# Kernel tuning notes

Hardware: AMD Instinct MI355X
Metric: run time of the kernel (lower is better)

The kernel has to match this reference:

```python
import jax, jax.numpy as jnp
import numpy as np

B, N, E, H, BS = 8, 8192, 256, 2, 8
D = E // H  # head_dim = 128


def setup_inputs() -> dict:
    key = jax.random.key(0)
    ks = jax.random.split(key, 8)
    s = 0.02
    return {
        "x": jax.random.normal(ks[0], (B, N, E), jnp.float32),
        "Wq": jax.random.normal(ks[1], (E, E), jnp.float32) * s,
        "bq": jnp.zeros((E,), jnp.float32),
        "Wk": jax.random.normal(ks[2], (E, E), jnp.float32) * s,
        "bk": jnp.zeros((E,), jnp.float32),
        "Wv": jax.random.normal(ks[3], (E, E), jnp.float32) * s,
        "bv": jnp.zeros((E,), jnp.float32),
        "P": jax.random.normal(ks[4], (D, D), jnp.float32) / jnp.sqrt(jnp.float32(D)),
    }


def reference(x, Wq, bq, Wk, bk, Wv, bv, P):
    Bx, Nx, Ex = x.shape
    nb = Nx // BS  # number of diagonal blocks
    # Linear projections (torch nn.Linear: y = x @ W^T + b), split heads
    q = (x @ Wq.T + bq).reshape(Bx, Nx, H, D)
    k = (x @ Wk.T + bk).reshape(Bx, Nx, H, D)
    v = (x @ Wv.T + bv).reshape(Bx, Nx, H, D)
    # Shared feature projection on q and k
    q = jnp.einsum('bnhe,ei->bnhi', q, P)
    k = jnp.einsum('bnhe,ei->bnhi', k, P)
    # Block-diagonal attention: off-block scores are -inf in the original,
    # so softmax over the full row == softmax within each block.
    qb = q.reshape(Bx, nb, BS, H, D)
    kb = k.reshape(Bx, nb, BS, H, D)
    vb = v.reshape(Bx, nb, BS, H, D)
    scores = jnp.einsum('bgnhd,bgmhd->bgnhm', qb, kb) / jnp.sqrt(jnp.asarray(D, x.dtype))
    attn = jax.nn.softmax(scores, axis=-1)  # [B, nb, BS, H, BS]
    out = jnp.einsum('bgnhm,bgmhd->bgnhd', attn, vb)
    return out.reshape(Bx, Nx, Ex)
```

## Files before the change

kernel.cpp:

```cpp
#include <hip/hip_runtime.h>


typedef __attribute__((ext_vector_type(8))) short bf16x8;
typedef __attribute__((ext_vector_type(4))) float f32x4;

__device__ __forceinline__ short f2bf(float f) {
  unsigned int u = __builtin_bit_cast(unsigned int, f);
  u = (u + 0x7FFFu + ((u >> 16) & 1u)) >> 16;
  return (short)u;
}
__device__ __forceinline__ float bf2f(short s) {
  unsigned int u = ((unsigned int)(unsigned short)s) << 16;
  return __builtin_bit_cast(float, u);
}
__device__ __forceinline__ int swz(int r) { return ((r ^ (r >> 3)) & 7) << 4; }

__global__ void prep_weights(const float* __restrict__ Wq, const float* __restrict__ bq,
                             const float* __restrict__ Wk, const float* __restrict__ bk,
                             const float* __restrict__ Wv, const float* __restrict__ bv,
                             const float* __restrict__ P,
                             short* __restrict__ WT, float* __restrict__ beff) {
  const int c = blockIdx.x;
  const int e = threadIdx.x;
  float acc = 0.f, bacc = 0.f;
  if (c < 512) {
    const float* W  = (c < 256) ? Wq : Wk;
    const float* bb = (c < 256) ? bq : bk;
    const int cc = c & 255;
    const int h = cc >> 7, i = cc & 127;
    for (int d = 0; d < 128; ++d) {
      const float p = P[d * 128 + i];
      acc += W[(h * 128 + d) * 256 + e] * p;
      if (e == 0) bacc += bb[h * 128 + d] * p;
    }
  } else {
    const int cc = c - 512;
    acc = Wv[cc * 256 + e];
    bacc = bv[cc];
  }
  WT[c * 256 + e] = f2bf(acc);
  if (e == 0) beff[c] = bacc;
}

__global__ __launch_bounds__(512, 4)
void fused_qkv_attn(const float* __restrict__ x, const short* __restrict__ WT,
                    const float* __restrict__ beff, float* __restrict__ out) {
  __shared__ __align__(16) char lds[65536];
  char* const xa = lds;
  char* const qk = lds + 16384;

  const int tid = threadIdx.x;
  const long tok0 = (long)blockIdx.x * 32;

  {
    const int r  = tid >> 4;
    const int kc = (tid & 15) * 16;
    const float4* xp = (const float4*)(x + (tok0 + r) * 256 + kc);
    float4 f0 = xp[0], f1 = xp[1], f2 = xp[2], f3 = xp[3];
    bf16x8 v0, v1;
    v0[0]=f2bf(f0.x); v0[1]=f2bf(f0.y); v0[2]=f2bf(f0.z); v0[3]=f2bf(f0.w);
    v0[4]=f2bf(f1.x); v0[5]=f2bf(f1.y); v0[6]=f2bf(f1.z); v0[7]=f2bf(f1.w);
    v1[0]=f2bf(f2.x); v1[1]=f2bf(f2.y); v1[2]=f2bf(f2.z); v1[3]=f2bf(f2.w);
    v1[4]=f2bf(f3.x); v1[5]=f2bf(f3.y); v1[6]=f2bf(f3.z); v1[7]=f2bf(f3.w);
    *(bf16x8*)(xa + r * 512 + ((kc * 2)       ^ swz(r))) = v0;
    *(bf16x8*)(xa + r * 512 + ((kc * 2 + 16)  ^ swz(r))) = v1;
  }
  __syncthreads();

  const int w = tid >> 6, l = tid & 63;
  const int lrow = l & 15, lk = l >> 4;
  const int nb = w * 96;

  f32x4 acc[2][6];
#pragma unroll
  for (int nf = 0; nf < 6; ++nf) {
    const float bv_ = beff[nb + nf * 16 + lrow];
    acc[0][nf] = (f32x4){bv_, bv_, bv_, bv_};
    acc[1][nf] = acc[0][nf];
  }
#pragma unroll
  for (int ks = 0; ks < 8; ++ks) {
    const int kb = ks * 32;
    bf16x8 a0 = *(const bf16x8*)(xa + lrow        * 512 + ((kb * 2 + lk * 16) ^ swz(lrow)));
    bf16x8 a1 = *(const bf16x8*)(xa + (16 + lrow) * 512 + ((kb * 2 + lk * 16) ^ swz(16 + lrow)));
#pragma unroll
    for (int nf = 0; nf < 6; ++nf) {
      const int col = nb + nf * 16 + lrow;
      bf16x8 b = *(const bf16x8*)(WT + col * 256 + kb + lk * 8);
      acc[0][nf] = __builtin_amdgcn_mfma_f32_16x16x32_bf16(a0, b, acc[0][nf], 0, 0, 0);
      acc[1][nf] = __builtin_amdgcn_mfma_f32_16x16x32_bf16(a1, b, acc[1][nf], 0, 0, 0);
    }
  }

#pragma unroll
  for (int mf = 0; mf < 2; ++mf)
#pragma unroll
    for (int nf = 0; nf < 6; ++nf)
#pragma unroll
      for (int r = 0; r < 4; ++r) {
        const int tok = mf * 16 + lk * 4 + r;
        const int c   = nb + nf * 16 + lrow;
        *(short*)(qk + tok * 1536 + ((c * 2) ^ swz(tok))) = f2bf(acc[mf][nf][r]);
      }
  __syncthreads();

  {
    const int blk = w >> 1, h = w & 1;
    const int i = l >> 3, j = l & 7;
    const int tq = blk * 8 + i, tk = blk * 8 + j;
    const int qc = h * 128, kcc = 256 + h * 128, vcc = 512 + h * 128;
    float s = 0.f;
#pragma unroll
    for (int dc = 0; dc < 16; ++dc) {
      bf16x8 qv = *(const bf16x8*)(qk + tq * 1536 + (((qc  + dc * 8) * 2) ^ swz(tq)));
      bf16x8 kv = *(const bf16x8*)(qk + tk * 1536 + (((kcc + dc * 8) * 2) ^ swz(tk)));
#pragma unroll
      for (int e = 0; e < 8; ++e) s += bf2f(qv[e]) * bf2f(kv[e]);
    }
    s *= 0.08838834764831843f;

    float mx = s;
    mx = fmaxf(mx, __shfl_xor(mx, 1, 8));
    mx = fmaxf(mx, __shfl_xor(mx, 2, 8));
    mx = fmaxf(mx, __shfl_xor(mx, 4, 8));
    const float p = __expf(s - mx);
    float sum = p;
    sum += __shfl_xor(sum, 1, 8);
    sum += __shfl_xor(sum, 2, 8);
    sum += __shfl_xor(sum, 4, 8);
    const float pn = p / sum;

    const int d0 = j * 16;
    float o[16];
#pragma unroll
    for (int c = 0; c < 16; ++c) o[c] = 0.f;
#pragma unroll
    for (int jj = 0; jj < 8; ++jj) {
      const float a = __shfl(pn, (l & 56) | jj, 64);
      const int tv = blk * 8 + jj;
      bf16x8 v0 = *(const bf16x8*)(qk + tv * 1536 + (((vcc + d0) * 2)     ^ swz(tv)));
      bf16x8 v1 = *(const bf16x8*)(qk + tv * 1536 + (((vcc + d0 + 8) * 2) ^ swz(tv)));
#pragma unroll
      for (int c = 0; c < 8; ++c) { o[c] += a * bf2f(v0[c]); o[8 + c] += a * bf2f(v1[c]); }
    }
    float4* op = (float4*)(out + (tok0 + tq) * 256 + h * 128 + d0);
    op[0] = (float4){o[0],  o[1],  o[2],  o[3]};
    op[1] = (float4){o[4],  o[5],  o[6],  o[7]};
    op[2] = (float4){o[8],  o[9],  o[10], o[11]};
    op[3] = (float4){o[12], o[13], o[14], o[15]};
  }
}

extern "C" void kernel_launch(void* const* d_in, const int* in_sizes, int n_in,
                              void* d_out, int out_size, void* d_ws, size_t ws_size,
                              hipStream_t stream) {
  const float* x  = (const float*)d_in[0];
  const float* Wq = (const float*)d_in[1];
  const float* bq = (const float*)d_in[2];
  const float* Wk = (const float*)d_in[3];
  const float* bk = (const float*)d_in[4];
  const float* Wv = (const float*)d_in[5];
  const float* bv = (const float*)d_in[6];
  const float* P  = (const float*)d_in[7];
  float* out = (float*)d_out;

  short* WT   = (short*)d_ws;
  float* beff = (float*)((char*)d_ws + 768 * 256 * 2);

  const int ntok = in_sizes[0] / 256;
  prep_weights<<<768, 256, 0, stream>>>(Wq, bq, Wk, bk, Wv, bv, P, WT, beff);
  fused_qkv_attn<<<ntok / 32, 512, 0, stream>>>(x, WT, beff, out);
}
```

Before: 229.3 us.

## Make fused kernel persistent over four tiles with double-buffered x prefetch

Each workgroup now processes four 32-token tiles in sequence. The next tile's x is loaded from global memory into registers during the current tile's MFMA work, then converted and written to a second LDS buffer. The MFMA operands are swapped so each lane holds four contiguous columns, which allows packed bf16 stores through v_cvt_pk_bf16_f32. The weight-prep kernel is also rewritten to use 80 blocks with P staged in LDS, and it converts Wv with vectorized loads. LDS use grows to 80KB and the grid shrinks fourfold, which may reduce occupancy and parallelism.

New measurement: 505.6 us. 120% more time.

```diff
diff --git a/kernel.cpp b/kernel.cpp
--- a/kernel.cpp
+++ b/kernel.cpp
@@ -3,6 +3,8 @@
 
 typedef __attribute__((ext_vector_type(8))) short bf16x8;
 typedef __attribute__((ext_vector_type(4))) float f32x4;
+typedef __attribute__((ext_vector_type(4))) unsigned int u32x4;
+typedef __attribute__((ext_vector_type(2))) unsigned int u32x2;
 
 __device__ __forceinline__ short f2bf(float f) {
   unsigned int u = __builtin_bit_cast(unsigned int, f);
@@ -13,141 +15,188 @@
   unsigned int u = ((unsigned int)(unsigned short)s) << 16;
   return __builtin_bit_cast(float, u);
 }
+__device__ __forceinline__ unsigned int cvtpk(float lo, float hi) {
+  unsigned int r;
+  asm("v_cvt_pk_bf16_f32 %0, %1, %2" : "=v"(r) : "v"(lo), "v"(hi));
+  return r;
+}
 __device__ __forceinline__ int swz(int r) { return ((r ^ (r >> 3)) & 7) << 4; }
 
-__global__ void prep_weights(const float* __restrict__ Wq, const float* __restrict__ bq,
-                             const float* __restrict__ Wk, const float* __restrict__ bk,
-                             const float* __restrict__ Wv, const float* __restrict__ bv,
-                             const float* __restrict__ P,
-                             short* __restrict__ WT, float* __restrict__ beff) {
-  const int c = blockIdx.x;
-  const int e = threadIdx.x;
-  float acc = 0.f, bacc = 0.f;
-  if (c < 512) {
-    const float* W  = (c < 256) ? Wq : Wk;
-    const float* bb = (c < 256) ? bq : bk;
-    const int cc = c & 255;
-    const int h = cc >> 7, i = cc & 127;
+__global__ void prep(const float* __restrict__ Wq, const float* __restrict__ bq,
+                     const float* __restrict__ Wk, const float* __restrict__ bk,
+                     const float* __restrict__ Wv, const float* __restrict__ bv,
+                     const float* __restrict__ P,
+                     short* __restrict__ WT, float* __restrict__ beff) {
+  __shared__ float Pl[128][8];
+  const int b = blockIdx.x, tid = threadIdx.x;
+  if (b < 64) {
+    const int m = b >> 5, h = (b >> 4) & 1, i0 = (b & 15) * 8;
+#pragma unroll
+    for (int it = 0; it < 4; ++it) {
+      const int idx = it * 256 + tid;
+      Pl[idx >> 3][idx & 7] = P[(idx >> 3) * 128 + i0 + (idx & 7)];
+    }
+    __syncthreads();
+    const float* __restrict__ W  = m ? Wk : Wq;
+    const float* __restrict__ bb = m ? bk : bq;
+    const int e = tid;
+    float acc[8] = {0.f, 0.f, 0.f, 0.f, 0.f, 0.f, 0.f, 0.f};
+#pragma unroll 4
     for (int d = 0; d < 128; ++d) {
-      const float p = P[d * 128 + i];
-      acc += W[(h * 128 + d) * 256 + e] * p;
-      if (e == 0) bacc += bb[h * 128 + d] * p;
+      const float wv = W[(h * 128 + d) * 256 + e];
+#pragma unroll
+      for (int ii = 0; ii < 8; ++ii) acc[ii] += wv * Pl[d][ii];
+    }
+#pragma unroll
+    for (int ii = 0; ii < 8; ++ii)
+      WT[(m * 256 + h * 128 + i0 + ii) * 256 + e] = f2bf(acc[ii]);
+    if (tid < 64) {
+      const int ii = tid & 7, dg = tid >> 3;
+      float p = 0.f;
+#pragma unroll
+      for (int dd = 0; dd < 16; ++dd) {
+        const int d = dg * 16 + dd;
+        p += bb[h * 128 + d] * Pl[d][ii];
+      }
+      p += __shfl_xor(p, 8);
+      p += __shfl_xor(p, 16);
+      p += __shfl_xor(p, 32);
+      if (tid < 8) beff[m * 256 + h * 128 + i0 + ii] = p;
     }
   } else {
-    const int cc = c - 512;
-    acc = Wv[cc * 256 + e];
-    bacc = bv[cc];
+    const int base = (b - 64) * 4096 + tid * 16;
+    const float4* vp = (const float4*)(Wv + base);
+    float4 f0 = vp[0], f1 = vp[1], f2 = vp[2], f3 = vp[3];
+    u32x4 v0 = { cvtpk(f0.x, f0.y), cvtpk(f0.z, f0.w), cvtpk(f1.x, f1.y), cvtpk(f1.z, f1.w) };
+    u32x4 v1 = { cvtpk(f2.x, f2.y), cvtpk(f2.z, f2.w), cvtpk(f3.x, f3.y), cvtpk(f3.z, f3.w) };
+    *(u32x4*)(WT + 512 * 256 + base)     = v0;
+    *(u32x4*)(WT + 512 * 256 + base + 8) = v1;
+    if (b == 64) beff[512 + tid] = bv[tid];
   }
-  WT[c * 256 + e] = f2bf(acc);
-  if (e == 0) beff[c] = bacc;
 }
 
 __global__ __launch_bounds__(512, 4)
 void fused_qkv_attn(const float* __restrict__ x, const short* __restrict__ WT,
                     const float* __restrict__ beff, float* __restrict__ out) {
-  __shared__ __align__(16) char lds[65536];
-  char* const xa = lds;
-  char* const qk = lds + 16384;
+  __shared__ __align__(16) char lds[81920];
+  char* const xaA = lds;
+  char* const xaB = lds + 16384;
+  char* const qk  = lds + 32768;
 
   const int tid = threadIdx.x;
-  const long tok0 = (long)blockIdx.x * 32;
-
-  {
-    const int r  = tid >> 4;
-    const int kc = (tid & 15) * 16;
-    const float4* xp = (const float4*)(x + (tok0 + r) * 256 + kc);
-    float4 f0 = xp[0], f1 = xp[1], f2 = xp[2], f3 = xp[3];
-    bf16x8 v0, v1;
-    v0[0]=f2bf(f0.x); v0[1]=f2bf(f0.y); v0[2]=f2bf(f0.z); v0[3]=f2bf(f0.w);
-    v0[4]=f2bf(f1.x); v0[5]=f2bf(f1.y); v0[6]=f2bf(f1.z); v0[7]=f2bf(f1.w);
-    v1[0]=f2bf(f2.x); v1[1]=f2bf(f2.y); v1[2]=f2bf(f2.z); v1[3]=f2bf(f2.w);
-    v1[4]=f2bf(f3.x); v1[5]=f2bf(f3.y); v1[6]=f2bf(f3.z); v1[7]=f2bf(f3.w);
-    *(bf16x8*)(xa + r * 512 + ((kc * 2)       ^ swz(r))) = v0;
-    *(bf16x8*)(xa + r * 512 + ((kc * 2 + 16)  ^ swz(r))) = v1;
-  }
-  __syncthreads();
-
   const int w = tid >> 6, l = tid & 63;
   const int lrow = l & 15, lk = l >> 4;
   const int nb = w * 96;
-
-  f32x4 acc[2][6];
-#pragma unroll
-  for (int nf = 0; nf < 6; ++nf) {
-    const float bv_ = beff[nb + nf * 16 + lrow];
-    acc[0][nf] = (f32x4){bv_, bv_, bv_, bv_};
-    acc[1][nf] = acc[0][nf];
+  const int sr = tid >> 4, skc = (tid & 15) * 16;
+
+  const long tile0 = (long)blockIdx.x * 4;
+
+  {
+    const float4* xp = (const float4*)(x + (tile0 * 32 + sr) * 256 + skc);
+    float4 f0 = xp[0], f1 = xp[1], f2 = xp[2], f3 = xp[3];
+    u32x4 v0 = { cvtpk(f0.x, f0.y), cvtpk(f0.z, f0.w), cvtpk(f1.x, f1.y), cvtpk(f1.z, f1.w) };
+    u32x4 v1 = { cvtpk(f2.x, f2.y), cvtpk(f2.z, f2.w), cvtpk(f3.x, f3.y), cvtpk(f3.z, f3.w) };
+    *(u32x4*)(xaA + sr * 512 + ((skc * 2)      ^ swz(sr))) = v0;
+    *(u32x4*)(xaA + sr * 512 + ((skc * 2 + 16) ^ swz(sr))) = v1;
   }
-#pragma unroll
-  for (int ks = 0; ks < 8; ++ks) {
-    const int kb = ks * 32;
-    bf16x8 a0 = *(const bf16x8*)(xa + lrow        * 512 + ((kb * 2 + lk * 16) ^ swz(lrow)));
-    bf16x8 a1 = *(const bf16x8*)(xa + (16 + lrow) * 512 + ((kb * 2 + lk * 16) ^ swz(16 + lrow)));
+
+  for (int t = 0; t < 4; ++t) {
+    char* const cur = (t & 1) ? xaB : xaA;
+    char* const nxt = (t & 1) ? xaA : xaB;
+    const long tok0 = (tile0 + t) * 32;
+    __syncthreads();
+
+    float4 pf0, pf1, pf2, pf3;
+    const bool pf = (t < 3);
+    if (pf) {
+      const float4* xp = (const float4*)(x + (tok0 + 32 + sr) * 256 + skc);
+      pf0 = xp[0]; pf1 = xp[1]; pf2 = xp[2]; pf3 = xp[3];
+    }
+
+    f32x4 acc[2][6];
 #pragma unroll
     for (int nf = 0; nf < 6; ++nf) {
-      const int col = nb + nf * 16 + lrow;
-      bf16x8 b = *(const bf16x8*)(WT + col * 256 + kb + lk * 8);
-      acc[0][nf] = __builtin_amdgcn_mfma_f32_16x16x32_bf16(a0, b, acc[0][nf], 0, 0, 0);
-      acc[1][nf] = __builtin_amdgcn_mfma_f32_16x16x32_bf16(a1, b, acc[1][nf], 0, 0, 0);
-    }
-  }
-
-#pragma unroll
-  for (int mf = 0; mf < 2; ++mf)
-#pragma unroll
-    for (int nf = 0; nf < 6; ++nf)
-#pragma unroll
-      for (int r = 0; r < 4; ++r) {
-        const int tok = mf * 16 + lk * 4 + r;
-        const int c   = nb + nf * 16 + lrow;
-        *(short*)(qk + tok * 1536 + ((c * 2) ^ swz(tok))) = f2bf(acc[mf][nf][r]);
-      }
-  __syncthreads();
-
-  {
-    const int blk = w >> 1, h = w & 1;
-    const int i = l >> 3, j = l & 7;
-    const int tq = blk * 8 + i, tk = blk * 8 + j;
-    const int qc = h * 128, kcc = 256 + h * 128, vcc = 512 + h * 128;
-    float s = 0.f;
-#pragma unroll
-    for (int dc = 0; dc < 16; ++dc) {
-      bf16x8 qv = *(const bf16x8*)(qk + tq * 1536 + (((qc  + dc * 8) * 2) ^ swz(tq)));
-      bf16x8 kv = *(const bf16x8*)(qk + tk * 1536 + (((kcc + dc * 8) * 2) ^ swz(tk)));
-#pragma unroll
-      for (int e = 0; e < 8; ++e) s += bf2f(qv[e]) * bf2f(kv[e]);
-    }
-    s *= 0.08838834764831843f;
-
-    float mx = s;
-    mx = fmaxf(mx, __shfl_xor(mx, 1, 8));
-    mx = fmaxf(mx, __shfl_xor(mx, 2, 8));
-    mx = fmaxf(mx, __shfl_xor(mx, 4, 8));
-    const float p = __expf(s - mx);
-    float sum = p;
-    sum += __shfl_xor(sum, 1, 8);
-    sum += __shfl_xor(sum, 2, 8);
-    sum += __shfl_xor(sum, 4, 8);
-    const float pn = p / sum;
-
-    const int d0 = j * 16;
-    float o[16];
-#pragma unroll
-    for (int c = 0; c < 16; ++c) o[c] = 0.f;
-#pragma unroll
-    for (int jj = 0; jj < 8; ++jj) {
-      const float a = __shfl(pn, (l & 56) | jj, 64);
-      const int tv = blk * 8 + jj;
-      bf16x8 v0 = *(const bf16x8*)(qk + tv * 1536 + (((vcc + d0) * 2)     ^ swz(tv)));
-      bf16x8 v1 = *(const bf16x8*)(qk + tv * 1536 + (((vcc + d0 + 8) * 2) ^ swz(tv)));
-#pragma unroll
-      for (int c = 0; c < 8; ++c) { o[c] += a * bf2f(v0[c]); o[8 + c] += a * bf2f(v1[c]); }
-    }
-    float4* op = (float4*)(out + (tok0 + tq) * 256 + h * 128 + d0);
-    op[0] = (float4){o[0],  o[1],  o[2],  o[3]};
-    op[1] = (float4){o[4],  o[5],  o[6],  o[7]};
-    op[2] = (float4){o[8],  o[9],  o[10], o[11]};
-    op[3] = (float4){o[12], o[13], o[14], o[15]};
+      f32x4 bi = *(const f32x4*)(beff + nb + nf * 16 + lk * 4);
+      acc[0][nf] = bi; acc[1][nf] = bi;
+    }
+#pragma unroll
+    for (int ks = 0; ks < 8; ++ks) {
+      const int kb = ks * 32;
+      bf16x8 xf0 = *(const bf16x8*)(cur + lrow * 512        + ((kb * 2 + lk * 16) ^ swz(lrow)));
+      bf16x8 xf1 = *(const bf16x8*)(cur + (16 + lrow) * 512 + ((kb * 2 + lk * 16) ^ swz(16 + lrow)));
+#pragma unroll
+      for (int nf = 0; nf < 6; ++nf) {
+        bf16x8 wf = *(const bf16x8*)(WT + (nb + nf * 16 + lrow) * 256 + kb + lk * 8);
+        acc[0][nf] = __builtin_amdgcn_mfma_f32_16x16x32_bf16(wf, xf0, acc[0][nf], 0, 0, 0);
+        acc[1][nf] = __builtin_amdgcn_mfma_f32_16x16x32_bf16(wf, xf1, acc[1][nf], 0, 0, 0);
+      }
+    }
+
+    if (pf) {
+      u32x4 v0 = { cvtpk(pf0.x, pf0.y), cvtpk(pf0.z, pf0.w), cvtpk(pf1.x, pf1.y), cvtpk(pf1.z, pf1.w) };
+      u32x4 v1 = { cvtpk(pf2.x, pf2.y), cvtpk(pf2.z, pf2.w), cvtpk(pf3.x, pf3.y), cvtpk(pf3.z, pf3.w) };
+      *(u32x4*)(nxt + sr * 512 + ((skc * 2)      ^ swz(sr))) = v0;
+      *(u32x4*)(nxt + sr * 512 + ((skc * 2 + 16) ^ swz(sr))) = v1;
+    }
+
+#pragma unroll
+    for (int mf = 0; mf < 2; ++mf) {
+      const int tok = mf * 16 + lrow;
+#pragma unroll
+      for (int nf = 0; nf < 6; ++nf) {
+        u32x2 pw = { cvtpk(acc[mf][nf][0], acc[mf][nf][1]),
+                     cvtpk(acc[mf][nf][2], acc[mf][nf][3]) };
+        const int colb = (nb + nf * 16 + lk * 4) * 2;
+        *(u32x2*)(qk + tok * 1536 + (colb ^ swz(tok))) = pw;
+      }
+    }
+    __syncthreads();
+
+    {
+      const int blk = w >> 1, h = w & 1;
+      const int i = l >> 3, j = l & 7;
+      const int tq = blk * 8 + i, tk = blk * 8 + j;
+      const int qc = h * 128, kcc = 256 + h * 128, vcc = 512 + h * 128;
+      float s = 0.f;
+#pragma unroll
+      for (int dc = 0; dc < 16; ++dc) {
+        bf16x8 qv = *(const bf16x8*)(qk + tq * 1536 + (((qc  + dc * 8) * 2) ^ swz(tq)));
+        bf16x8 kv = *(const bf16x8*)(qk + tk * 1536 + (((kcc + dc * 8) * 2) ^ swz(tk)));
+#pragma unroll
+        for (int e = 0; e < 8; ++e) s += bf2f(qv[e]) * bf2f(kv[e]);
+      }
+      s *= 0.08838834764831843f;
+
+      float mx = s;
+      mx = fmaxf(mx, __shfl_xor(mx, 1, 8));
+      mx = fmaxf(mx, __shfl_xor(mx, 2, 8));
+      mx = fmaxf(mx, __shfl_xor(mx, 4, 8));
+      const float p = __expf(s - mx);
+      float sum = p;
+      sum += __shfl_xor(sum, 1, 8);
+      sum += __shfl_xor(sum, 2, 8);
+      sum += __shfl_xor(sum, 4, 8);
+      const float pn = p / sum;
+
+      const int d0 = j * 16;
+      float o[16];
+#pragma unroll
+      for (int c = 0; c < 16; ++c) o[c] = 0.f;
+#pragma unroll
+      for (int jj = 0; jj < 8; ++jj) {
+        const float a = __shfl(pn, (l & 56) | jj, 64);
+        const int tv = blk * 8 + jj;
+        bf16x8 v0 = *(const bf16x8*)(qk + tv * 1536 + (((vcc + d0) * 2)     ^ swz(tv)));
+        bf16x8 v1 = *(const bf16x8*)(qk + tv * 1536 + (((vcc + d0 + 8) * 2) ^ swz(tv)));
+#pragma unroll
+        for (int c = 0; c < 8; ++c) { o[c] += a * bf2f(v0[c]); o[8 + c] += a * bf2f(v1[c]); }
+      }
+      float4* op = (float4*)(out + (tok0 + tq) * 256 + h * 128 + d0);
+      op[0] = (float4){o[0],  o[1],  o[2],  o[3]};
+      op[1] = (float4){o[4],  o[5],  o[6],  o[7]};
+      op[2] = (float4){o[8],  o[9],  o[10], o[11]};
+      op[3] = (float4){o[12], o[13], o[14], o[15]};
+    }
   }
 }
 
@@ -168,6 +217,6 @@
   float* beff = (float*)((char*)d_ws + 768 * 256 * 2);
 
   const int ntok = in_sizes[0] / 256;
-  prep_weights<<<768, 256, 0, stream>>>(Wq, bq, Wk, bk, Wv, bv, P, WT, beff);
-  fused_qkv_attn<<<ntok / 32, 512, 0, stream>>>(x, WT, beff, out);
-}
+  prep<<<80, 256, 0, stream>>>(Wq, bq, Wk, bk, Wv, bv, P, WT, beff);
+  fused_qkv_attn<<<ntok / (32 * 4), 512, 0, stream>>>(x, WT, beff, out);
+}
```
